# Optimization experiments

Hardware: AMD Instinct MI355X
Metric: run time of the kernel (lower is better)

Reference implementation:

```python
import jax, jax.numpy as jnp
import numpy as np
from jax import lax

E, BANDS, T, NCLS, TOPK, DBN = 62, 5, 64, 4, 10, 32
NODE_DIM = 512  # 128 channels * 4 width after conv-pool chain


def _conv(x, w, b):
    # x: (N,C,H,W), w: (O,I,kh,kw) torch layout
    y = lax.conv_general_dilated(x, w, window_strides=(1, 1), padding='VALID',
                                 dimension_numbers=('NCHW', 'OIHW', 'NCHW'))
    return y + b[None, :, None, None]


def _maxpool_1x2(x):
    return lax.reduce_window(x, -jnp.inf, lax.max, (1, 1, 1, 2), (1, 1, 1, 2), 'VALID')


def _sogc(H, W_bn, gc_w, gc_b, k):
    # H: (B,E,Din). Dropout omitted (eval mode).
    G = jnp.tanh(jnp.einsum('bed,kd->bek', H, W_bn))            # (B,E,DBN)
    A = jax.nn.softmax(jnp.einsum('bek,bfk->bef', G, G), axis=-1)  # (B,E,E)
    vals, idxs = lax.top_k(A, k)                                  # (B,E,k)
    B = H.shape[0]
    bi = jnp.arange(B)[:, None, None]
    ei = jnp.arange(H.shape[1])[None, :, None]
    A_sparse = jnp.zeros_like(A).at[bi, ei, idxs].set(vals)
    M = jnp.einsum('bef,bfd->bed', A_sparse, H)                   # (B,E,Din)
    return jax.nn.relu(jnp.einsum('bed,od->beo', M, gc_w) + gc_b)


def setup_inputs() -> dict:
    key = jax.random.key(0)
    ks = jax.random.split(key, 20)
    r = lambda i, shape, s: (jax.random.normal(ks[i], shape, dtype=jnp.float32) * s)
    B = 512
    return {
        'x': r(0, (B, E, BANDS, T), 1.0),
        'conv1_w': r(1, (32, 1, 5, 5), 0.2), 'conv1_b': r(2, (32,), 0.02),
        'conv2_w': r(3, (64, 32, 1, 5), 0.08), 'conv2_b': r(4, (64,), 0.02),
        'conv3_w': r(5, (128, 64, 1, 5), 0.06), 'conv3_b': r(6, (128,), 0.02),
        'Wbn1': r(7, (DBN, NODE_DIM), 0.04),
        'gc1_w': r(8, (64, NODE_DIM), 0.04), 'gc1_b': r(9, (64,), 0.02),
        'Wbn2': r(10, (DBN, 64), 0.12),
        'gc2_w': r(11, (64, 64), 0.12), 'gc2_b': r(12, (64,), 0.02),
        'Wbn3': r(13, (DBN, 64), 0.12),
        'gc3_w': r(14, (64, 64), 0.12), 'gc3_b': r(15, (64,), 0.02),
        'cls_w': r(16, (NCLS, E * 64), 0.02), 'cls_b': r(17, (NCLS,), 0.02),
    }


def reference(x, conv1_w, conv1_b, conv2_w, conv2_b, conv3_w, conv3_b,
              Wbn1, gc1_w, gc1_b, Wbn2, gc2_w, gc2_b, Wbn3, gc3_w, gc3_b,
              cls_w, cls_b):
    B = x.shape[0]
    h = x.reshape(B * E, 1, BANDS, T)
    h = _maxpool_1x2(jax.nn.relu(_conv(h, conv1_w, conv1_b)))  # (BE,32,1,30)
    h = _maxpool_1x2(jax.nn.relu(_conv(h, conv2_w, conv2_b)))  # (BE,64,1,13)
    h = _maxpool_1x2(jax.nn.relu(_conv(h, conv3_w, conv3_b)))  # (BE,128,1,4)
    h = h.reshape(B, E, NODE_DIM)
    h = _sogc(h, Wbn1, gc1_w, gc1_b, TOPK)
    h = _sogc(h, Wbn2, gc2_w, gc2_b, TOPK)
    h = _sogc(h, Wbn3, gc3_w, gc3_b, TOPK)
    logits = h.reshape(B, E * 64) @ cls_w.T + cls_b
    return logits
```

## Files before the change

### kernel.cpp

```cpp
#include <hip/hip_runtime.h>

#define E_NODES 62
#define TOPK 10

__global__ __launch_bounds__(256) void wt_kernel(
    const float* __restrict__ w2, const float* __restrict__ w3,
    float* __restrict__ w2t, float* __restrict__ w3t)
{
  const int j = blockIdx.x * 256 + threadIdx.x;
  if (j < 10240) {
    const int r = j >> 6, o = j & 63;
    w2t[j] = w2[o * 160 + r];
  } else {
    const int k = j - 10240;
    const int r = k >> 7, o = k & 127;
    w3t[k] = w3[o * 320 + r];
  }
}

__device__ __forceinline__ void stage_async(const float* __restrict__ g,
                                            float* l, int n, int tid) {
  for (int i = tid; i < n; i += 256)
    __builtin_amdgcn_global_load_lds(
        (const __attribute__((address_space(1))) void*)(g + i),
        (__attribute__((address_space(3))) void*)(l + i), 4, 0, 0);
}


__global__ __launch_bounds__(256, 3) void conv_chain_kernel(
    const float* __restrict__ x,
    const float* __restrict__ w1, const float* __restrict__ b1,
    const float* __restrict__ w2t, const float* __restrict__ b2,
    const float* __restrict__ w3t, const float* __restrict__ b3,
    float* __restrict__ H3)
{
  __shared__ float sm[13312];
  float* s_h1  = sm;
  float* s_h2  = sm + 4096;
  float* s_wa  = sm + 8192;
  float* s_wb  = sm + 10752;
  float* s_w1  = sm + 8192;
  float* s_img = sm + 9024;

  const int tid = threadIdx.x;
  const int n0 = blockIdx.x * 4;
  const int im = tid >> 6;
  const int lane = tid & 63;

  stage_async(x + (size_t)n0 * 320, s_img, 1280, tid);
  for (int i = tid; i < 832; i += 256) s_w1[i] = (i < 800) ? w1[i] : b1[i - 800];
  __syncthreads();

  stage_async(w2t, s_wb, 2560, tid);

  {
    const int tp = lane & 31;
    const int half = lane >> 5;
    if (tp < 30) {
      const float* ib = s_img + im * 320;
      const int t0 = 2 * tp;
      float r[5][6];
#pragma unroll
      for (int kr = 0; kr < 5; ++kr)
#pragma unroll
        for (int c = 0; c < 6; ++c) r[kr][c] = ib[kr * 64 + t0 + c];
#pragma unroll 4
      for (int oi = 0; oi < 16; ++oi) {
        const int o = half * 16 + oi;
        const float* w = s_w1 + o * 25;
        float s0 = s_w1[800 + o], s1 = s0;
#pragma unroll
        for (int kr = 0; kr < 5; ++kr) {
#pragma unroll
          for (int k = 0; k < 5; ++k) {
            const float wv = w[kr * 5 + k];
            s0 += r[kr][k] * wv;
            s1 += r[kr][k + 1] * wv;
          }
        }
        s_h1[im * 1024 + o * 32 + tp] = fmaxf(fmaxf(s0, s1), 0.f);
      }
    }
  }
  __syncthreads();

  {
    const int o = lane;
    const float bia = b2[o];

    {
      float acc0[7], acc1[7];
#pragma unroll
      for (int t = 0; t < 7; ++t) { acc0[t] = bia; acc1[t] = bia; }
#pragma unroll 1
      for (int c = 0; c < 4; ++c) {
        const float* rb = (c & 1) ? s_wa : s_wb;
        float*       nb = (c & 1) ? s_wb : s_wa;
        stage_async(w2t + ((c < 3) ? (c + 1) * 2560 : 0), nb, 2560, tid);
#pragma unroll 4
        for (int cl = 0; cl < 8; ++cl) {
          const float* hr = s_h1 + im * 1024 + (c * 8 + cl) * 32;
          float r[18];
#pragma unroll
          for (int q = 0; q < 4; ++q) {
            const float4 v = *(const float4*)(hr + q * 4);
            r[q * 4] = v.x; r[q * 4 + 1] = v.y; r[q * 4 + 2] = v.z; r[q * 4 + 3] = v.w;
          }
          { const float2 v = *(const float2*)(hr + 16); r[16] = v.x; r[17] = v.y; }
          const float* wb = rb + cl * 320 + o;
#pragma unroll
          for (int k = 0; k < 5; ++k) {
            const float wv = wb[k * 64];
#pragma unroll
            for (int t = 0; t < 7; ++t) {
              acc0[t] += r[2 * t + k] * wv;
              acc1[t] += r[2 * t + 1 + k] * wv;
            }
          }
        }
        __syncthreads();
      }
#pragma unroll
      for (int t = 0; t < 7; ++t)
        s_h2[im * 1024 + o * 16 + t] = fmaxf(fmaxf(acc0[t], acc1[t]), 0.f);
    }

    {
      float acc0[6], acc1[6];
#pragma unroll
      for (int t = 0; t < 6; ++t) { acc0[t] = bia; acc1[t] = bia; }
#pragma unroll 1
      for (int c = 0; c < 4; ++c) {
        const float* rb = (c & 1) ? s_wa : s_wb;
        float*       nb = (c & 1) ? s_wb : s_wa;
        stage_async((c < 3) ? (w2t + (c + 1) * 2560) : w3t, nb, 2560, tid);
#pragma unroll 4
        for (int cl = 0; cl < 8; ++cl) {
          const float* hr = s_h1 + im * 1024 + (c * 8 + cl) * 32;
          float r[18];
#pragma unroll
          for (int q = 0; q < 4; ++q) {
            const float4 v = *(const float4*)(hr + 12 + q * 4);
            r[q * 4] = v.x; r[q * 4 + 1] = v.y; r[q * 4 + 2] = v.z; r[q * 4 + 3] = v.w;
          }
          { const float2 v = *(const float2*)(hr + 28); r[16] = v.x; r[17] = v.y; }
          const float* wb = rb + cl * 320 + o;
#pragma unroll
          for (int k = 0; k < 5; ++k) {
            const float wv = wb[k * 64];
#pragma unroll
            for (int t = 0; t < 6; ++t) {
              const int t0 = 2 * t + 2;
              acc0[t] += r[t0 + k] * wv;
              acc1[t] += r[t0 + 1 + k] * wv;
            }
          }
        }
        __syncthreads();
      }
#pragma unroll
      for (int t = 0; t < 6; ++t)
        s_h2[im * 1024 + o * 16 + 7 + t] = fmaxf(fmaxf(acc0[t], acc1[t]), 0.f);
    }
  }

  {
    const int oc = lane;
    float acc[2][8];
#pragma unroll
    for (int t = 0; t < 8; ++t) {
      acc[0][t] = b3[oc];
      acc[1][t] = b3[64 + oc];
    }
#pragma unroll 1
    for (int k = 0; k < 16; ++k) {
      const float* rb = (k & 1) ? s_wa : s_wb;
      float*       nb = (k & 1) ? s_wb : s_wa;
      if (k < 15) stage_async(w3t + (k + 1) * 2560, nb, 2560, tid);
#pragma unroll 2
      for (int cl = 0; cl < 4; ++cl) {
        const float* hr = s_h2 + im * 1024 + (k * 4 + cl) * 16;
        float r[12];
#pragma unroll
        for (int q = 0; q < 3; ++q) {
          const float4 v = *(const float4*)(hr + q * 4);
          r[q * 4] = v.x; r[q * 4 + 1] = v.y; r[q * 4 + 2] = v.z; r[q * 4 + 3] = v.w;
        }
        const float* wb = rb + cl * 640 + oc;
#pragma unroll
        for (int kk = 0; kk < 5; ++kk) {
          const float wv0 = wb[kk * 128];
          const float wv1 = wb[kk * 128 + 64];
#pragma unroll
          for (int t = 0; t < 8; ++t) {
            acc[0][t] += r[t + kk] * wv0;
            acc[1][t] += r[t + kk] * wv1;
          }
        }
      }
      __syncthreads();
    }
    float* hout = H3 + (size_t)(n0 + im) * 512;
    float4 ov;
    ov.x = fmaxf(fmaxf(acc[0][0], acc[0][1]), 0.f);
    ov.y = fmaxf(fmaxf(acc[0][2], acc[0][3]), 0.f);
    ov.z = fmaxf(fmaxf(acc[0][4], acc[0][5]), 0.f);
    ov.w = fmaxf(fmaxf(acc[0][6], acc[0][7]), 0.f);
    *(float4*)(hout + oc * 4) = ov;
    ov.x = fmaxf(fmaxf(acc[1][0], acc[1][1]), 0.f);
    ov.y = fmaxf(fmaxf(acc[1][2], acc[1][3]), 0.f);
    ov.z = fmaxf(fmaxf(acc[1][4], acc[1][5]), 0.f);
    ov.w = fmaxf(fmaxf(acc[1][6], acc[1][7]), 0.f);
    *(float4*)(hout + (64 + oc) * 4) = ov;
  }
}

__global__ __launch_bounds__(256) void gp_kernel(
    const float* __restrict__ H3, const float* __restrict__ Wbn1,
    const float* __restrict__ gc1w, float* __restrict__ GP)
{
  __shared__ float sH[32 * 65];
  __shared__ float sW[96 * 65];
  const int tid = threadIdx.x;
  const int n0 = blockIdx.x * 32;
  const int im = tid >> 3;
  const int oq = tid & 7;

  float acc[12];
#pragma unroll
  for (int j = 0; j < 12; ++j) acc[j] = 0.f;

#pragma unroll 1
  for (int c8 = 0; c8 < 8; ++c8) {
    const int d0 = c8 * 64;
    __syncthreads();
    for (int i = tid; i < 2048; i += 256) {
      const int r = i >> 6, cc = i & 63;
      sH[r * 65 + cc] = H3[(size_t)(n0 + r) * 512 + d0 + cc];
    }
    for (int i = tid; i < 6144; i += 256) {
      const int o = i >> 6, cc = i & 63;
      sW[o * 65 + cc] = (o < 32) ? Wbn1[o * 512 + d0 + cc]
                                 : gc1w[(o - 32) * 512 + d0 + cc];
    }
    __syncthreads();
#pragma unroll 4
    for (int d = 0; d < 64; ++d) {
      const float h = sH[im * 65 + d];
#pragma unroll
      for (int j = 0; j < 12; ++j)
        acc[j] += h * sW[(oq * 12 + j) * 65 + d];
    }
  }
  float* gpo = GP + (size_t)(n0 + im) * 96;
#pragma unroll
  for (int j = 0; j < 12; ++j) {
    const int o = oq * 12 + j;
    gpo[o] = (o < 32) ? (1.f - 2.f / (__expf(2.f * acc[j]) + 1.f)) : acc[j];
  }
}

__global__ __launch_bounds__(256) void sogc1_kernel(
    const float* __restrict__ GP, const float* __restrict__ gcb,
    float* __restrict__ Hout)
{
  __shared__ float sG[62 * 33];
  __shared__ float sP[62 * 64];
  __shared__ float stv[620];
  __shared__ int   sti[620];
  const int b = blockIdx.x, tid = threadIdx.x;
  const int lane = tid & 63, wave = tid >> 6;

  const float* gp = GP + (size_t)b * 62 * 96;
  for (int i = tid; i < 62 * 96; i += 256) {
    const int e = i / 96, q = i - e * 96;
    const float v = gp[i];
    if (q < 32) sG[e * 33 + q] = v; else sP[e * 64 + (q - 32)] = v;
  }
  __syncthreads();

  for (int e = wave; e < E_NODES; e += 4) {
    float sc = -1e30f;
    if (lane < E_NODES) {
      float s = 0.f;
#pragma unroll
      for (int k = 0; k < 32; ++k) s += sG[e * 33 + k] * sG[lane * 33 + k];
      sc = s;
    }
    float mx = sc;
#pragma unroll
    for (int off = 32; off; off >>= 1) mx = fmaxf(mx, __shfl_xor(mx, off));
    float p = (lane < E_NODES) ? __expf(sc - mx) : 0.f;
    float sum = p;
#pragma unroll
    for (int off = 32; off; off >>= 1) sum += __shfl_xor(sum, off);
    p = p / sum;
    float v = (lane < E_NODES) ? p : -1.f;
#pragma unroll 1
    for (int it = 0; it < TOPK; ++it) {
      float bv = v; int bi = lane;
#pragma unroll
      for (int off = 32; off; off >>= 1) {
        const float ov = __shfl_xor(bv, off);
        const int   oi = __shfl_xor(bi, off);
        if (ov > bv || (ov == bv && oi < bi)) { bv = ov; bi = oi; }
      }
      if (lane == 0) { stv[e * 10 + it] = bv; sti[e * 10 + it] = bi; }
      if (lane == bi) v = -1.f;
    }
  }
  __syncthreads();

  for (int e = wave; e < E_NODES; e += 4) {
    float acc = gcb[lane];
#pragma unroll
    for (int j = 0; j < TOPK; ++j)
      acc += stv[e * 10 + j] * sP[sti[e * 10 + j] * 64 + lane];
    Hout[((size_t)b * E_NODES + e) * 64 + lane] = fmaxf(acc, 0.f);
  }
}

template <bool CLS>
__global__ __launch_bounds__(256) void sogc64_kernel(
    const float* __restrict__ Hin, const float* __restrict__ Wbn,
    const float* __restrict__ gcw, const float* __restrict__ gcb,
    const float* __restrict__ cw, const float* __restrict__ cb,
    float* __restrict__ outbuf)
{
  extern __shared__ float sm[];
  float* sH  = sm;
  float* sWt = sm + 4030;
  float* sG  = sm + 10238;
  float* sP  = sm + 12284;
  float* stv = sm + 16252;
  int*   sti = (int*)(sm + 16872);
  float* sred = sm + 17492;

  const int b = blockIdx.x, tid = threadIdx.x;
  const int lane = tid & 63, wave = tid >> 6;

  const float* Hb = Hin + (size_t)b * 62 * 64;
  for (int i = tid; i < 62 * 64; i += 256)
    sH[(i >> 6) * 65 + (i & 63)] = Hb[i];
  for (int i = tid; i < 64 * 64; i += 256)
    sWt[(i & 63) * 97 + (i >> 6)] = gcw[i];
  for (int i = tid; i < 32 * 64; i += 256)
    sWt[(i & 63) * 97 + 64 + (i >> 6)] = Wbn[i];
  __syncthreads();

  for (int e = wave; e < E_NODES; e += 4) {
    const float* hrow = sH + e * 65;
    const float* wp = sWt + lane;
    const float* wg = sWt + 64 + (lane & 31);
    float accp = 0.f, accg = 0.f;
#pragma unroll 8
    for (int d = 0; d < 64; ++d) {
      const float h = hrow[d];
      accp += h * wp[d * 97];
      accg += h * wg[d * 97];
    }
    sP[e * 64 + lane] = accp;
    if (lane < 32) sG[e * 33 + lane] = 1.f - 2.f / (__expf(2.f * accg) + 1.f);
  }
  __syncthreads();

  for (int e = wave; e < E_NODES; e += 4) {
    float sc = -1e30f;
    if (lane < E_NODES) {
      float s = 0.f;
#pragma unroll
      for (int k = 0; k < 32; ++k) s += sG[e * 33 + k] * sG[lane * 33 + k];
      sc = s;
    }
    float mx = sc;
#pragma unroll
    for (int off = 32; off; off >>= 1) mx = fmaxf(mx, __shfl_xor(mx, off));
    float p = (lane < E_NODES) ? __expf(sc - mx) : 0.f;
    float sum = p;
#pragma unroll
    for (int off = 32; off; off >>= 1) sum += __shfl_xor(sum, off);
    p = p / sum;
    float v = (lane < E_NODES) ? p : -1.f;
#pragma unroll 1
    for (int it = 0; it < TOPK; ++it) {
      float bv = v; int bi = lane;
#pragma unroll
      for (int off = 32; off; off >>= 1) {
        const float ov = __shfl_xor(bv, off);
        const int   oi = __shfl_xor(bi, off);
        if (ov > bv || (ov == bv && oi < bi)) { bv = ov; bi = oi; }
      }
      if (lane == 0) { stv[e * 10 + it] = bv; sti[e * 10 + it] = bi; }
      if (lane == bi) v = -1.f;
    }
  }
  __syncthreads();

  float accn[4] = {0.f, 0.f, 0.f, 0.f};
  for (int e = wave; e < E_NODES; e += 4) {
    float acc = gcb[lane];
#pragma unroll
    for (int j = 0; j < TOPK; ++j)
      acc += stv[e * 10 + j] * sP[sti[e * 10 + j] * 64 + lane];
    acc = fmaxf(acc, 0.f);
    if (CLS) {
#pragma unroll
      for (int n = 0; n < 4; ++n)
        accn[n] += acc * cw[n * 3968 + e * 64 + lane];
    } else {
      outbuf[((size_t)b * E_NODES + e) * 64 + lane] = acc;
    }
  }
  if (CLS) {
#pragma unroll
    for (int n = 0; n < 4; ++n) {
      float s = accn[n];
#pragma unroll
      for (int off = 32; off; off >>= 1) s += __shfl_xor(s, off);
      if (lane == 0) sred[wave * 4 + n] = s;
    }
    __syncthreads();
    if (tid < 4)
      outbuf[b * 4 + tid] = cb[tid] + sred[tid] + sred[4 + tid] + sred[8 + tid] + sred[12 + tid];
  }
}

extern "C" void kernel_launch(void* const* d_in, const int* in_sizes, int n_in,
                              void* d_out, int out_size, void* d_ws, size_t ws_size,
                              hipStream_t stream) {
  const float* x    = (const float*)d_in[0];
  const float* c1w  = (const float*)d_in[1];
  const float* c1b  = (const float*)d_in[2];
  const float* c2w  = (const float*)d_in[3];
  const float* c2b  = (const float*)d_in[4];
  const float* c3w  = (const float*)d_in[5];
  const float* c3b  = (const float*)d_in[6];
  const float* Wbn1 = (const float*)d_in[7];
  const float* gc1w = (const float*)d_in[8];
  const float* gc1b = (const float*)d_in[9];
  const float* Wbn2 = (const float*)d_in[10];
  const float* gc2w = (const float*)d_in[11];
  const float* gc2b = (const float*)d_in[12];
  const float* Wbn3 = (const float*)d_in[13];
  const float* gc3w = (const float*)d_in[14];
  const float* gc3b = (const float*)d_in[15];
  const float* clsw = (const float*)d_in[16];
  const float* clsb = (const float*)d_in[17];
  float* out = (float*)d_out;

  float* wsf = (float*)d_ws;
  float* W2T = wsf;
  float* W3T = wsf + 10240;
  float* H3  = wsf + 51200;
  float* GP  = H3 + (size_t)16252928;
  float* Hs1 = GP + (size_t)3047424;
  float* Hs2 = Hs1 + (size_t)2031616;

  const int SOGC64_BYTES = 17508 * 4;

  (void)hipFuncSetAttribute((const void*)sogc64_kernel<false>,
                            hipFuncAttributeMaxDynamicSharedMemorySize, SOGC64_BYTES);
  (void)hipFuncSetAttribute((const void*)sogc64_kernel<true>,
                            hipFuncAttributeMaxDynamicSharedMemorySize, SOGC64_BYTES);

  wt_kernel<<<200, 256, 0, stream>>>(c2w, c3w, W2T, W3T);
  conv_chain_kernel<<<7936, 256, 0, stream>>>(x, c1w, c1b, W2T, c2b, W3T, c3b, H3);
  gp_kernel<<<992, 256, 0, stream>>>(H3, Wbn1, gc1w, GP);
  sogc1_kernel<<<512, 256, 0, stream>>>(GP, gc1b, Hs1);
  sogc64_kernel<false><<<512, 256, SOGC64_BYTES, stream>>>(
      Hs1, Wbn2, gc2w, gc2b, nullptr, nullptr, Hs2);
  sogc64_kernel<true><<<512, 256, SOGC64_BYTES, stream>>>(
      Hs2, Wbn3, gc3w, gc3b, clsw, clsb, out);
}
```

Baseline: 1.178 ms.

## Fuse first SOGC projection into conv chain and widen async LDS staging to 16 bytes

Removes the separate gp_kernel. The conv chain now keeps each node's 512-wide feature vector in shared memory and immediately projects it against a pre-transposed Wbn1/gc1 weight matrix, streamed in double-buffered chunks. This avoids writing and re-reading the large H3 intermediate in global memory. Async global-to-LDS staging also switches from 4-byte to 16-byte transfers, cutting the number of load instructions. The cost is extra weight streaming and extra syncs per conv block (96 outputs by 512 inputs for every 4 nodes), which repeats weight traffic that gp_kernel had amortized over 32 nodes.

```diff
diff --git a/kernel.cpp b/kernel.cpp
--- a/kernel.cpp
+++ b/kernel.cpp
@@ -5,25 +5,32 @@
 
 __global__ __launch_bounds__(256) void wt_kernel(
     const float* __restrict__ w2, const float* __restrict__ w3,
-    float* __restrict__ w2t, float* __restrict__ w3t)
+    const float* __restrict__ Wbn1, const float* __restrict__ gc1w,
+    float* __restrict__ w2t, float* __restrict__ w3t, float* __restrict__ wt)
 {
   const int j = blockIdx.x * 256 + threadIdx.x;
   if (j < 10240) {
     const int r = j >> 6, o = j & 63;
     w2t[j] = w2[o * 160 + r];
-  } else {
+  } else if (j < 51200) {
     const int k = j - 10240;
     const int r = k >> 7, o = k & 127;
     w3t[k] = w3[o * 320 + r];
-  }
-}
-
-__device__ __forceinline__ void stage_async(const float* __restrict__ g,
-                                            float* l, int n, int tid) {
-  for (int i = tid; i < n; i += 256)
+  } else {
+    const int k = j - 51200;
+    const int d4 = k / 384, rem = k - d4 * 384;
+    const int jj = rem >> 2, q = rem & 3;
+    const int d = d4 * 4 + q;
+    wt[k] = (jj < 32) ? Wbn1[jj * 512 + d] : gc1w[(jj - 32) * 512 + d];
+  }
+}
+
+__device__ __forceinline__ void stage16(const float* __restrict__ g,
+                                        float* l, int n4, int tid) {
+  for (int i = tid; i < n4; i += 256)
     __builtin_amdgcn_global_load_lds(
-        (const __attribute__((address_space(1))) void*)(g + i),
-        (__attribute__((address_space(3))) void*)(l + i), 4, 0, 0);
+        (const __attribute__((address_space(1))) void*)(g + 4 * i),
+        (__attribute__((address_space(3))) void*)(l + 4 * i), 16, 0, 0);
 }
 
 
@@ -32,7 +39,7 @@
     const float* __restrict__ w1, const float* __restrict__ b1,
     const float* __restrict__ w2t, const float* __restrict__ b2,
     const float* __restrict__ w3t, const float* __restrict__ b3,
-    float* __restrict__ H3)
+    const float* __restrict__ WT, float* __restrict__ GP)
 {
   __shared__ float sm[13312];
   float* s_h1  = sm;
@@ -47,11 +54,11 @@
   const int im = tid >> 6;
   const int lane = tid & 63;
 
-  stage_async(x + (size_t)n0 * 320, s_img, 1280, tid);
+  stage16(x + (size_t)n0 * 320, s_img, 320, tid);
   for (int i = tid; i < 832; i += 256) s_w1[i] = (i < 800) ? w1[i] : b1[i - 800];
   __syncthreads();
 
-  stage_async(w2t, s_wb, 2560, tid);
+  stage16(w2t, s_wb, 640, tid);
 
   {
     const int tp = lane & 31;
@@ -96,7 +103,7 @@
       for (int c = 0; c < 4; ++c) {
         const float* rb = (c & 1) ? s_wa : s_wb;
         float*       nb = (c & 1) ? s_wb : s_wa;
-        stage_async(w2t + ((c < 3) ? (c + 1) * 2560 : 0), nb, 2560, tid);
+        stage16(w2t + ((c < 3) ? (c + 1) * 2560 : 0), nb, 640, tid);
 #pragma unroll 4
         for (int cl = 0; cl < 8; ++cl) {
           const float* hr = s_h1 + im * 1024 + (c * 8 + cl) * 32;
@@ -133,7 +140,7 @@
       for (int c = 0; c < 4; ++c) {
         const float* rb = (c & 1) ? s_wa : s_wb;
         float*       nb = (c & 1) ? s_wb : s_wa;
-        stage_async((c < 3) ? (w2t + (c + 1) * 2560) : w3t, nb, 2560, tid);
+        stage16((c < 3) ? (w2t + (c + 1) * 2560) : w3t, nb, 640, tid);
 #pragma unroll 4
         for (int cl = 0; cl < 8; ++cl) {
           const float* hr = s_h1 + im * 1024 + (c * 8 + cl) * 32;
@@ -164,6 +171,8 @@
     }
   }
 
+  stage16(WT, s_h1, 768, tid);
+
   {
     const int oc = lane;
     float acc[2][8];
@@ -176,7 +185,7 @@
     for (int k = 0; k < 16; ++k) {
       const float* rb = (k & 1) ? s_wa : s_wb;
       float*       nb = (k & 1) ? s_wb : s_wa;
-      if (k < 15) stage_async(w3t + (k + 1) * 2560, nb, 2560, tid);
+      if (k < 15) stage16(w3t + (k + 1) * 2560, nb, 640, tid);
 #pragma unroll 2
       for (int cl = 0; cl < 4; ++cl) {
         const float* hr = s_h2 + im * 1024 + (k * 4 + cl) * 16;
@@ -200,63 +209,43 @@
       }
       __syncthreads();
     }
-    float* hout = H3 + (size_t)(n0 + im) * 512;
+    float* h3w = s_wb + im * 520;
     float4 ov;
     ov.x = fmaxf(fmaxf(acc[0][0], acc[0][1]), 0.f);
     ov.y = fmaxf(fmaxf(acc[0][2], acc[0][3]), 0.f);
     ov.z = fmaxf(fmaxf(acc[0][4], acc[0][5]), 0.f);
     ov.w = fmaxf(fmaxf(acc[0][6], acc[0][7]), 0.f);
-    *(float4*)(hout + oc * 4) = ov;
+    *(float4*)(h3w + oc * 4) = ov;
     ov.x = fmaxf(fmaxf(acc[1][0], acc[1][1]), 0.f);
     ov.y = fmaxf(fmaxf(acc[1][2], acc[1][3]), 0.f);
     ov.z = fmaxf(fmaxf(acc[1][4], acc[1][5]), 0.f);
     ov.w = fmaxf(fmaxf(acc[1][6], acc[1][7]), 0.f);
-    *(float4*)(hout + (64 + oc) * 4) = ov;
-  }
-}
-
-__global__ __launch_bounds__(256) void gp_kernel(
-    const float* __restrict__ H3, const float* __restrict__ Wbn1,
-    const float* __restrict__ gc1w, float* __restrict__ GP)
-{
-  __shared__ float sH[32 * 65];
-  __shared__ float sW[96 * 65];
-  const int tid = threadIdx.x;
-  const int n0 = blockIdx.x * 32;
-  const int im = tid >> 3;
-  const int oq = tid & 7;
-
-  float acc[12];
-#pragma unroll
-  for (int j = 0; j < 12; ++j) acc[j] = 0.f;
-
-#pragma unroll 1
-  for (int c8 = 0; c8 < 8; ++c8) {
-    const int d0 = c8 * 64;
+    *(float4*)(h3w + 256 + oc * 4) = ov;
+  }
+
+  {
+    stage16(WT + 3072, s_h2, 768, tid);
     __syncthreads();
-    for (int i = tid; i < 2048; i += 256) {
-      const int r = i >> 6, cc = i & 63;
-      sH[r * 65 + cc] = H3[(size_t)(n0 + r) * 512 + d0 + cc];
-    }
-    for (int i = tid; i < 6144; i += 256) {
-      const int o = i >> 6, cc = i & 63;
-      sW[o * 65 + cc] = (o < 32) ? Wbn1[o * 512 + d0 + cc]
-                                 : gc1w[(o - 32) * 512 + d0 + cc];
-    }
-    __syncthreads();
-#pragma unroll 4
-    for (int d = 0; d < 64; ++d) {
-      const float h = sH[im * 65 + d];
-#pragma unroll
-      for (int j = 0; j < 12; ++j)
-        acc[j] += h * sW[(oq * 12 + j) * 65 + d];
-    }
-  }
-  float* gpo = GP + (size_t)(n0 + im) * 96;
-#pragma unroll
-  for (int j = 0; j < 12; ++j) {
-    const int o = oq * 12 + j;
-    gpo[o] = (o < 32) ? (1.f - 2.f / (__expf(2.f * acc[j]) + 1.f)) : acc[j];
+    const float* h3 = s_wb + im * 520;
+    const int jP = 32 + lane, jG = lane & 31;
+    float accp = 0.f, accg = 0.f;
+#pragma unroll 1
+    for (int s = 0; s < 16; ++s) {
+      const float* z = (s & 1) ? s_h2 : s_h1;
+#pragma unroll
+      for (int d4 = 0; d4 < 8; ++d4) {
+        const float4 hv = *(const float4*)(h3 + s * 32 + d4 * 4);
+        const float4 wp = *(const float4*)(z + d4 * 384 + jP * 4);
+        const float4 wg = *(const float4*)(z + d4 * 384 + jG * 4);
+        accp += hv.x * wp.x + hv.y * wp.y + hv.z * wp.z + hv.w * wp.w;
+        accg += hv.x * wg.x + hv.y * wg.y + hv.z * wg.z + hv.w * wg.w;
+      }
+      __syncthreads();
+      if (s < 14) stage16(WT + (s + 2) * 3072, (s & 1) ? s_h2 : s_h1, 768, tid);
+    }
+    float* gpo = GP + (size_t)(n0 + im) * 96;
+    gpo[32 + lane] = accp;
+    if (lane < 32) gpo[lane] = 1.f - 2.f / (__expf(2.f * accg) + 1.f);
   }
 }
 
@@ -451,8 +440,8 @@
   float* wsf = (float*)d_ws;
   float* W2T = wsf;
   float* W3T = wsf + 10240;
-  float* H3  = wsf + 51200;
-  float* GP  = H3 + (size_t)16252928;
+  float* WT  = wsf + 51200;
+  float* GP  = wsf + 100352;
   float* Hs1 = GP + (size_t)3047424;
   float* Hs2 = Hs1 + (size_t)2031616;
 
@@ -463,9 +452,9 @@
   (void)hipFuncSetAttribute((const void*)sogc64_kernel<true>,
                             hipFuncAttributeMaxDynamicSharedMemorySize, SOGC64_BYTES);
 
-  wt_kernel<<<200, 256, 0, stream>>>(c2w, c3w, W2T, W3T);
-  conv_chain_kernel<<<7936, 256, 0, stream>>>(x, c1w, c1b, W2T, c2b, W3T, c3b, H3);
-  gp_kernel<<<992, 256, 0, stream>>>(H3, Wbn1, gc1w, GP);
+  wt_kernel<<<392, 256, 0, stream>>>(c2w, c3w, Wbn1, gc1w, W2T, W3T, WT);
+  conv_chain_kernel<<<7936, 256, 0, stream>>>(x, c1w, c1b, W2T, c2b, W3T, c3b,
+                                              WT, GP);
   sogc1_kernel<<<512, 256, 0, stream>>>(GP, gc1b, Hs1);
   sogc64_kernel<false><<<512, 256, SOGC64_BYTES, stream>>>(
       Hs1, Wbn2, gc2w, gc2b, nullptr, nullptr, Hs2);
```

Measured after the change: 1.167 ms. No clear change (-1.0%).
